# Optimization experiments

Measured on AMD Instinct MI355X. Metric: run time of the kernel, lower is better.

Reference implementation:

```python
import math
import jax, jax.numpy as jnp
import numpy as np

D_MODEL = 1024
NUM_HEADS = 16
HEAD_DIM = D_MODEL // NUM_HEADS
B, T = 2, 2048


def setup_inputs() -> dict:
    key = jax.random.key(0)
    ks = jax.random.split(key, 11)
    s = 0.02
    inp = {
        'x':  jax.random.normal(ks[0], (B, T, D_MODEL), dtype=jnp.float32),
        'Wq': jax.random.normal(ks[1], (D_MODEL, D_MODEL), dtype=jnp.float32) * s,
        'bq': jax.random.normal(ks[2], (D_MODEL,), dtype=jnp.float32) * s,
        'Wk': jax.random.normal(ks[3], (D_MODEL, D_MODEL), dtype=jnp.float32) * s,
        'bk': jax.random.normal(ks[4], (D_MODEL,), dtype=jnp.float32) * s,
        'Wv': jax.random.normal(ks[5], (D_MODEL, D_MODEL), dtype=jnp.float32) * s,
        'bv': jax.random.normal(ks[6], (D_MODEL,), dtype=jnp.float32) * s,
        'Wt': jax.random.normal(ks[7], (D_MODEL, D_MODEL), dtype=jnp.float32) * s,
        'bt': jax.random.normal(ks[8], (D_MODEL,), dtype=jnp.float32) * s,
        'Wo': jax.random.normal(ks[9], (D_MODEL, D_MODEL), dtype=jnp.float32) * s,
        'bo': jax.random.normal(ks[10], (D_MODEL,), dtype=jnp.float32) * s,
    }
    return inp


def reference(x, Wq, bq, Wk, bk, Wv, bv, Wt, bt, Wo, bo):
    Bx, Tx, D = x.shape
    H, hd = NUM_HEADS, HEAD_DIM
    scale = 1.0 / math.sqrt(hd)

    def proj(W, b):
        # (B,T,D) -> (B,H,T,hd); torch Linear uses x @ W.T + b
        return (x @ W.T + b).reshape(Bx, Tx, H, hd).transpose(0, 2, 1, 3)

    q = proj(Wq, bq)
    k = proj(Wk, bk)
    v = proj(Wv, bv)
    t = proj(Wt, bt)

    # dot-product term: (B,H,T,T)
    scores = jnp.einsum('bhqd,bhkd->bhqk', q, k)
    # triplet term: cumsum over key positions of (k*v)/sqrt(hd)
    kv_cumsum = jnp.cumsum(k * v * scale, axis=2)  # (B,H,T,hd)
    scores = scores + jnp.einsum('bhqd,bhkd->bhqk', q * t, kv_cumsum)
    scores = scores * scale

    # causal mask: position j > i forbidden
    causal = jnp.tril(jnp.ones((Tx, Tx), dtype=bool))
    scores = jnp.where(causal[None, None], scores, jnp.float32(-jnp.inf))

    attn = jax.nn.softmax(scores, axis=-1)  # stable max-subtract internally
    out = jnp.einsum('bhqk,bhkd->bhqd', attn, v)
    out = out.transpose(0, 2, 1, 3).reshape(Bx, Tx, D)
    return out @ Wo.T + bo
```

## Files before the change

kernel.cpp:

```cpp
#include <hip/hip_runtime.h>
#include <hip/hip_bf16.h>

typedef unsigned short u16;
typedef __attribute__((ext_vector_type(8))) short bf16x8;
typedef __attribute__((ext_vector_type(4))) float f32x4;
typedef __attribute__((ext_vector_type(4))) unsigned int u32x4;

#define LOG2E 1.44269504088896340736f

static __device__ __forceinline__ float b2f(u16 u) {
    union { float f; unsigned int i; } v; v.i = ((unsigned int)u) << 16; return v.f;
}
static __device__ __forceinline__ u16 f2b(float f) {
    unsigned int x = __builtin_bit_cast(unsigned int, f);
    unsigned int r = (x + 0x7fffu + ((x >> 16) & 1u)) >> 16;
    return (u16)r;
}
static __device__ __forceinline__ void gll16(const u16* g, u16* l) {
    __builtin_amdgcn_global_load_lds((const __attribute__((address_space(1))) void*)g,
                                     (__attribute__((address_space(3))) void*)l, 16, 0, 0);
}
static __device__ __forceinline__ float fexp2(float x) {
    float r; asm("v_exp_f32 %0, %1" : "=v"(r) : "v"(x)); return r;
}

__global__ __launch_bounds__(256) void cvt_all(const float* __restrict__ x,
                                               const float* __restrict__ w0, const float* __restrict__ w1,
                                               const float* __restrict__ w2, const float* __restrict__ w3,
                                               const float* __restrict__ w4, u16* __restrict__ dst) {
    size_t c = (size_t)blockIdx.x * 256 + threadIdx.x;
    size_t e = c * 4;
    const float* s; size_t off;
    const size_t M4 = (size_t)4 << 20, M1 = (size_t)1 << 20;
    if (e < M4) { s = x; off = e; }
    else {
        size_t r = e - M4; int wsel = (int)(r >> 20); off = r & (M1 - 1);
        s = wsel == 0 ? w0 : wsel == 1 ? w1 : wsel == 2 ? w2 : wsel == 3 ? w3 : w4;
    }
    float4 v = *(const float4*)(s + off);
    u16* d = dst + e;
    d[0] = f2b(v.x); d[1] = f2b(v.y); d[2] = f2b(v.z); d[3] = f2b(v.w);
}

static __device__ __forceinline__ void gemm_body(const u16* __restrict__ A, const u16* __restrict__ W,
                                                 const float* __restrict__ bias, void* __restrict__ outp,
                                                 int mode, u16* Al, u16* Bl) {
    const int tid = threadIdx.x, lane = tid & 63, w = tid >> 6;
    const int wr = w >> 1, wc = w & 1;
    const int l15 = lane & 15, lhi = lane >> 4;
    const int tm = blockIdx.y * 128, tn = blockIdx.x * 128;

    f32x4 acc[4][4] = {};

    for (int kt = 0; kt < 16; ++kt) {
        const int k0 = kt * 64;
        for (int i = 0; i < 4; ++i) {
            int rl = i * 32 + w * 8 + (lane >> 3);
            int c  = (lane & 7) ^ (rl & 7);
            gll16(A + (size_t)(tm + rl) * 1024 + k0 + c * 8, Al + (i * 32 + w * 8) * 64);
            gll16(W + (size_t)(tn + rl) * 1024 + k0 + c * 8, Bl + (i * 32 + w * 8) * 64);
        }
        __syncthreads();
        for (int ks = 0; ks < 2; ++ks) {
            bf16x8 af[4], bfr[4];
            for (int mi = 0; mi < 4; ++mi) {
                int row = wr * 64 + mi * 16 + l15;
                int cc = (ks * 4 + lhi) ^ (row & 7);
                af[mi] = *(const bf16x8*)(Al + row * 64 + cc * 8);
            }
            for (int ni = 0; ni < 4; ++ni) {
                int row = wc * 64 + ni * 16 + l15;
                int cc = (ks * 4 + lhi) ^ (row & 7);
                bfr[ni] = *(const bf16x8*)(Bl + row * 64 + cc * 8);
            }
            for (int mi = 0; mi < 4; ++mi)
                for (int ni = 0; ni < 4; ++ni)
                    acc[mi][ni] = __builtin_amdgcn_mfma_f32_16x16x32_bf16(af[mi], bfr[ni], acc[mi][ni], 0, 0, 0);
        }
        __syncthreads();
    }

    float bcol[4];
    for (int ni = 0; ni < 4; ++ni) bcol[ni] = bias[tn + wc * 64 + ni * 16 + l15];

    for (int mi = 0; mi < 4; ++mi)
        for (int ni = 0; ni < 4; ++ni)
            for (int r = 0; r < 4; ++r) {
                int rg = tm + wr * 64 + mi * 16 + lhi * 4 + r;
                int cg = tn + wc * 64 + ni * 16 + l15;
                float v = acc[mi][ni][r] + bcol[ni];
                if (mode == 2) {
                    ((float*)outp)[(size_t)rg * 1024 + cg] = v;
                } else {
                    int b = rg >> 11, t = rg & 2047, h = cg >> 6, d = cg & 63;
                    if (mode == 0)
                        ((u16*)outp)[(((size_t)(b * 16 + h)) * 2048 + t) * 128 + d] = f2b(v);
                    else
                        ((u16*)outp)[(((size_t)(b * 16 + h)) * 2048 + t) * 64 + d] = f2b(v);
                }
            }
}

__global__ __launch_bounds__(256) void gemm_bt(const u16* __restrict__ A, const u16* __restrict__ W,
                                               const float* __restrict__ bias, void* __restrict__ outp,
                                               int mode) {
    __shared__ u16 Al[128 * 64];
    __shared__ u16 Bl[128 * 64];
    gemm_body(A, W, bias, outp, mode, Al, Bl);
}

struct ProjArgs {
    const u16* W[4];
    const float* b[4];
    u16* out[4];
};

__global__ __launch_bounds__(256) void gemm_proj(const u16* __restrict__ A, ProjArgs pa) {
    __shared__ u16 Al[128 * 64];
    __shared__ u16 Bl[128 * 64];
    const int z = blockIdx.z;
    gemm_body(A, pa.W[z], pa.b[z], pa.out[z], (z < 2) ? 0 : 1, Al, Bl);
}

__global__ __launch_bounds__(256) void qt_mul(u16* __restrict__ Qa, const u16* __restrict__ Tp) {
    int idx = blockIdx.x * 256 + threadIdx.x;
    int tg = idx >> 3, dc = idx & 7;
    bf16x8 q = *(const bf16x8*)(Qa + (size_t)tg * 128 + dc * 8);
    bf16x8 tt = *(const bf16x8*)(Tp + (size_t)tg * 64 + dc * 8);
    bf16x8 o;
    #pragma unroll
    for (int j = 0; j < 8; ++j) o[j] = (short)f2b(b2f((u16)q[j]) * b2f((u16)tt[j]));
    *(bf16x8*)(Qa + (size_t)tg * 128 + 64 + dc * 8) = o;
}

__global__ __launch_bounds__(256) void transpose_v(const u16* __restrict__ V, u16* __restrict__ VT) {
    __shared__ u16 tile[64][72];
    const int bh = blockIdx.y, tc = blockIdx.x;
    const u16* Vh = V + ((size_t)bh * 2048 + tc * 64) * 64;
    u16* VTh = VT + (size_t)bh * 64 * 2048 + tc * 64;
    const int tid = threadIdx.x;
    for (int i = 0; i < 2; ++i) {
        int f = i * 256 + tid;
        int r = f >> 3, dc = f & 7;
        bf16x8 v = *(const bf16x8*)(Vh + r * 64 + dc * 8);
        #pragma unroll
        for (int j = 0; j < 8; ++j) tile[dc * 8 + j][r] = (u16)v[j];
    }
    __syncthreads();
    for (int i = 0; i < 2; ++i) {
        int f = i * 256 + tid;
        int d = f >> 3, t8 = (f & 7) * 8;
        bf16x8 o;
        #pragma unroll
        for (int j = 0; j < 8; ++j) {
            int pos = t8 + j;
            int key = (pos & 32) + 16 * ((pos >> 2) & 1) + 4 * ((pos >> 3) & 3) + (pos & 3);
            o[j] = (short)tile[d][key];
        }
        *(bf16x8*)(VTh + (size_t)d * 2048 + t8) = o;
    }
}

__global__ __launch_bounds__(256) void cumsum_kv(u16* __restrict__ Ka, const u16* __restrict__ V) {
    const int bh = blockIdx.x, dg = blockIdx.y;
    u16* Kh = Ka + (size_t)bh * 2048 * 128;
    const u16* Vh = V + (size_t)bh * 2048 * 64;
    const int d16 = threadIdx.x & 15, c = threadIdx.x >> 4;
    const int d = dg * 16 + d16;
    __shared__ float sums[16][17];
    float s = 0.f;
    for (int i = 0; i < 128; ++i) {
        int t = c * 128 + i;
        s += b2f(Kh[t * 128 + d]) * b2f(Vh[t * 64 + d]);
    }
    sums[c][d16] = s;
    __syncthreads();
    float run = 0.f;
    for (int cc = 0; cc < c; ++cc) run += sums[cc][d16];
    for (int i = 0; i < 128; ++i) {
        int t = c * 128 + i;
        run += b2f(Kh[t * 128 + d]) * b2f(Vh[t * 64 + d]);
        Kh[t * 128 + 64 + d] = f2b(run * 0.125f);
    }
}

__global__ __launch_bounds__(256, 3) void attn5(const u16* __restrict__ Qa, const u16* __restrict__ Ka,
                                                const u16* __restrict__ VT, u16* __restrict__ Obuf) {
    const int wg = blockIdx.x;
    const int xcd = wg & 7, slot = wg >> 3;
    const int bh = xcd * 4 + (slot >> 4);
    const int qp = slot & 15;
    const int tiL = qp, tiH = 31 - qp;
    const int q0L = tiL * 64, q0H = tiH * 64;
    const int NT = tiH + 1;
    const u16* Qh = Qa + (size_t)bh * 2048 * 128;
    const u16* Kh = Ka + (size_t)bh * 2048 * 128;
    const u16* VTh = VT + (size_t)bh * 64 * 2048;

    __shared__ u16 Kl[2][64 * 128];
    __shared__ u16 Vl[2][64 * 64];

    const int tid = threadIdx.x, lane = tid & 63, w = tid >> 6;
    const int l15 = lane & 15, lhi = lane >> 4;
    const float SC = 0.125f * LOG2E;

    bf16x8 qfL[4], qfH[4];
    #pragma unroll
    for (int ks = 0; ks < 4; ++ks) {
        bf16x8 a = *(const bf16x8*)(Qh + (size_t)(q0L + w * 16 + l15) * 128 + ks * 32 + lhi * 8);
        bf16x8 b = *(const bf16x8*)(Qh + (size_t)(q0H + w * 16 + l15) * 128 + ks * 32 + lhi * 8);
        bf16x8 oa, ob;
        #pragma unroll
        for (int j = 0; j < 8; ++j) {
            oa[j] = (short)f2b(b2f((u16)a[j]) * SC);
            ob[j] = (short)f2b(b2f((u16)b[j]) * SC);
        }
        qfL[ks] = oa; qfH[ks] = ob;
    }

    f32x4 accL[4] = {}, accH[4] = {};
    float lsL = 0.f, lsH = 0.f;

    auto STAGE = [&](int buf, int ti) {
        const int kv0 = ti * 64;
        #pragma unroll
        for (int i = 0; i < 4; ++i) {
            int lr = i * 16 + w * 4 + lhi;
            int c = l15 ^ (lr & 15);
            gll16(Kh + (size_t)(kv0 + lr) * 128 + c * 8, &Kl[buf][(i * 16 + w * 4) * 128]);
        }
        #pragma unroll
        for (int i = 0; i < 2; ++i) {
            int dr = i * 32 + w * 8 + (lane >> 3);
            int c = (lane & 7) ^ (dr & 7);
            gll16(VTh + (size_t)dr * 2048 + kv0 + c * 8, &Vl[buf][(i * 32 + w * 8) * 64]);
        }
    };

    STAGE(0, 0);
    asm volatile("s_waitcnt vmcnt(0)" ::: "memory");
    __builtin_amdgcn_s_barrier();

    for (int ti = 0; ti < NT; ++ti) {
        const int cur = ti & 1;
        if (ti + 1 < NT) STAGE(cur ^ 1, ti + 1);
        const bool doL = (ti <= tiL);

        f32x4 sH[4] = {}, sL[4] = {};
        #pragma unroll
        for (int ks = 0; ks < 4; ++ks) {
            bf16x8 kf[4];
            #pragma unroll
            for (int k2 = 0; k2 < 4; ++k2) {
                int kl = k2 * 16 + l15;
                int cc = (ks * 4 + lhi) ^ l15;
                kf[k2] = *(const bf16x8*)(&Kl[cur][kl * 128 + cc * 8]);
            }
            __builtin_amdgcn_s_setprio(1);
            #pragma unroll
            for (int k2 = 0; k2 < 4; ++k2)
                sH[k2] = __builtin_amdgcn_mfma_f32_16x16x32_bf16(kf[k2], qfH[ks], sH[k2], 0, 0, 0);
            if (doL) {
                #pragma unroll
                for (int k2 = 0; k2 < 4; ++k2)
                    sL[k2] = __builtin_amdgcn_mfma_f32_16x16x32_bf16(kf[k2], qfL[ks], sL[k2], 0, 0, 0);
            }
            __builtin_amdgcn_s_setprio(0);
        }

        auto FINISH = [&](f32x4* sacc, f32x4* acc, float& lsum, bool diag) {
            float p[4][4];
            #pragma unroll
            for (int k2 = 0; k2 < 4; ++k2)
                #pragma unroll
                for (int r = 0; r < 4; ++r) {
                    float s = sacc[k2][r];
                    if (diag) {
                        int key = k2 * 16 + lhi * 4 + r;
                        int qq = w * 16 + l15;
                        s = (key <= qq) ? s : -1e30f;
                    }
                    float pe = fexp2(s);
                    p[k2][r] = pe;
                    lsum += pe;
                }
            bf16x8 pf[2];
            #pragma unroll
            for (int ks2 = 0; ks2 < 2; ++ks2) {
                unsigned int w0, w1, w2, w3;
                asm("v_cvt_pk_bf16_f32 %0, %1, %2" : "=v"(w0) : "v"(p[2 * ks2][0]),     "v"(p[2 * ks2][1]));
                asm("v_cvt_pk_bf16_f32 %0, %1, %2" : "=v"(w1) : "v"(p[2 * ks2][2]),     "v"(p[2 * ks2][3]));
                asm("v_cvt_pk_bf16_f32 %0, %1, %2" : "=v"(w2) : "v"(p[2 * ks2 + 1][0]), "v"(p[2 * ks2 + 1][1]));
                asm("v_cvt_pk_bf16_f32 %0, %1, %2" : "=v"(w3) : "v"(p[2 * ks2 + 1][2]), "v"(p[2 * ks2 + 1][3]));
                u32x4 t = {w0, w1, w2, w3};
                pf[ks2] = __builtin_bit_cast(bf16x8, t);
            }
            #pragma unroll
            for (int ks2 = 0; ks2 < 2; ++ks2) {
                __builtin_amdgcn_s_setprio(1);
                #pragma unroll
                for (int dt = 0; dt < 4; ++dt) {
                    int dd = dt * 16 + l15;
                    int cc = (ks2 * 4 + lhi) ^ (dd & 7);
                    bf16x8 vf = *(const bf16x8*)(&Vl[cur][dd * 64 + cc * 8]);
                    acc[dt] = __builtin_amdgcn_mfma_f32_16x16x32_bf16(pf[ks2], vf, acc[dt], 0, 0, 0);
                }
                __builtin_amdgcn_s_setprio(0);
            }
        };

        FINISH(sH, accH, lsH, ti == tiH);
        if (doL) FINISH(sL, accL, lsL, ti == tiL);

        asm volatile("s_waitcnt vmcnt(0)" ::: "memory");
        __builtin_amdgcn_s_barrier();
    }

    lsH += __shfl_xor(lsH, 16, 64); lsH += __shfl_xor(lsH, 32, 64);
    lsL += __shfl_xor(lsL, 16, 64); lsL += __shfl_xor(lsL, 32, 64);
    float invH[4], invL[4];
    #pragma unroll
    for (int r = 0; r < 4; ++r) {
        invH[r] = 1.0f / __shfl(lsH, lhi * 4 + r, 64);
        invL[r] = 1.0f / __shfl(lsL, lhi * 4 + r, 64);
    }
    #pragma unroll
    for (int dt = 0; dt < 4; ++dt)
        #pragma unroll
        for (int r = 0; r < 4; ++r) {
            int cr = lhi * 4 + r;
            int dd = dt * 16 + l15;
            int qgL = q0L + w * 16 + cr;
            int qgH = q0H + w * 16 + cr;
            size_t nL = (size_t)(bh >> 4) * 2048 + qgL;
            size_t nH = (size_t)(bh >> 4) * 2048 + qgH;
            Obuf[nL * 1024 + (bh & 15) * 64 + dd] = f2b(accL[dt][r] * invL[r]);
            Obuf[nH * 1024 + (bh & 15) * 64 + dd] = f2b(accH[dt][r] * invH[r]);
        }
}

extern "C" void kernel_launch(void* const* d_in, const int* in_sizes, int n_in,
                              void* d_out, int out_size, void* d_ws, size_t ws_size,
                              hipStream_t stream) {
    (void)in_sizes; (void)n_in; (void)out_size; (void)ws_size;
    const float* x  = (const float*)d_in[0];
    const float* Wq = (const float*)d_in[1];
    const float* bq = (const float*)d_in[2];
    const float* Wk = (const float*)d_in[3];
    const float* bk = (const float*)d_in[4];
    const float* Wv = (const float*)d_in[5];
    const float* bv = (const float*)d_in[6];
    const float* Wt = (const float*)d_in[7];
    const float* bt = (const float*)d_in[8];
    const float* Wo = (const float*)d_in[9];
    const float* bo = (const float*)d_in[10];

    const size_t M1 = 1024u * 1024u;
    u16* xb   = (u16*)d_ws;
    u16* wq   = xb + 4 * M1;
    u16* wk   = wq + M1;
    u16* wv   = wk + M1;
    u16* wt   = wv + M1;
    u16* wo   = wt + M1;
    u16* Qa   = wo + M1;
    u16* Kaa  = Qa + 8 * M1;
    u16* Vtm  = Kaa + 8 * M1;
    u16* Ttm  = Vtm + 4 * M1;
    u16* Obuf = Ttm + 4 * M1;
    u16* VTg  = Ttm;

    cvt_all<<<9216, 256, 0, stream>>>(x, Wq, Wk, Wv, Wt, Wo, xb);

    ProjArgs pa;
    pa.W[0] = wq; pa.W[1] = wk; pa.W[2] = wv; pa.W[3] = wt;
    pa.b[0] = bq; pa.b[1] = bk; pa.b[2] = bv; pa.b[3] = bt;
    pa.out[0] = Qa; pa.out[1] = Kaa; pa.out[2] = Vtm; pa.out[3] = Ttm;
    gemm_proj<<<dim3(8, 32, 4), 256, 0, stream>>>(xb, pa);

    qt_mul<<<2048, 256, 0, stream>>>(Qa, Ttm);
    transpose_v<<<dim3(32, 32), 256, 0, stream>>>(Vtm, VTg);
    cumsum_kv<<<dim3(32, 4), 256, 0, stream>>>(Kaa, Vtm);

    attn5<<<512, 256, 0, stream>>>(Qa, Kaa, VTg, Obuf);

    gemm_bt<<<dim3(8, 32), 256, 0, stream>>>(Obuf, wo, bo, d_out, 2);
}
```

Before: 158.1 us.

## Split attention into 32-row query pairs with 2-wave blocks, load V directly to registers

The attention kernel moves from 4-wave blocks handling paired 64-row query tiles to 2-wave blocks handling paired 32-row tiles, doubling the grid to 1024 blocks. V fragments are now read straight from global memory into registers each tile instead of being staged through LDS, and the wait/barrier is adjusted to allow partial vmcnt overlap. The output projection now uses a 64x128 tile, giving twice as many blocks. The aim is better CU occupancy and load balance on this small problem, at the cost of more redundant K loads per query row and uncoalesced V reads.

```diff
diff --git a/kernel.cpp b/kernel.cpp
--- a/kernel.cpp
+++ b/kernel.cpp
@@ -42,38 +42,50 @@
     d[0] = f2b(v.x); d[1] = f2b(v.y); d[2] = f2b(v.z); d[3] = f2b(v.w);
 }
 
+template<int WM>
 static __device__ __forceinline__ void gemm_body(const u16* __restrict__ A, const u16* __restrict__ W,
                                                  const float* __restrict__ bias, void* __restrict__ outp,
                                                  int mode, u16* Al, u16* Bl) {
     const int tid = threadIdx.x, lane = tid & 63, w = tid >> 6;
     const int wr = w >> 1, wc = w & 1;
     const int l15 = lane & 15, lhi = lane >> 4;
-    const int tm = blockIdx.y * 128, tn = blockIdx.x * 128;
-
-    f32x4 acc[4][4] = {};
+    const int tm = blockIdx.y * (WM * 32), tn = blockIdx.x * 128;
+
+    f32x4 acc[WM][4] = {};
 
     for (int kt = 0; kt < 16; ++kt) {
         const int k0 = kt * 64;
+        #pragma unroll
+        for (int i = 0; i < WM; ++i) {
+            int rl = i * 32 + w * 8 + (lane >> 3);
+            int c  = (lane & 7) ^ (rl & 7);
+            gll16(A + (size_t)(tm + rl) * 1024 + k0 + c * 8, Al + (i * 32 + w * 8) * 64);
+        }
+        #pragma unroll
         for (int i = 0; i < 4; ++i) {
             int rl = i * 32 + w * 8 + (lane >> 3);
             int c  = (lane & 7) ^ (rl & 7);
-            gll16(A + (size_t)(tm + rl) * 1024 + k0 + c * 8, Al + (i * 32 + w * 8) * 64);
             gll16(W + (size_t)(tn + rl) * 1024 + k0 + c * 8, Bl + (i * 32 + w * 8) * 64);
         }
         __syncthreads();
+        #pragma unroll
         for (int ks = 0; ks < 2; ++ks) {
-            bf16x8 af[4], bfr[4];
-            for (int mi = 0; mi < 4; ++mi) {
-                int row = wr * 64 + mi * 16 + l15;
+            bf16x8 af[WM], bfr[4];
+            #pragma unroll
+            for (int mi = 0; mi < WM; ++mi) {
+                int row = wr * (WM * 16) + mi * 16 + l15;
                 int cc = (ks * 4 + lhi) ^ (row & 7);
                 af[mi] = *(const bf16x8*)(Al + row * 64 + cc * 8);
             }
+            #pragma unroll
             for (int ni = 0; ni < 4; ++ni) {
                 int row = wc * 64 + ni * 16 + l15;
                 int cc = (ks * 4 + lhi) ^ (row & 7);
                 bfr[ni] = *(const bf16x8*)(Bl + row * 64 + cc * 8);
             }
-            for (int mi = 0; mi < 4; ++mi)
+            #pragma unroll
+            for (int mi = 0; mi < WM; ++mi)
+                #pragma unroll
                 for (int ni = 0; ni < 4; ++ni)
                     acc[mi][ni] = __builtin_amdgcn_mfma_f32_16x16x32_bf16(af[mi], bfr[ni], acc[mi][ni], 0, 0, 0);
         }
@@ -81,12 +93,16 @@
     }
 
     float bcol[4];
+    #pragma unroll
     for (int ni = 0; ni < 4; ++ni) bcol[ni] = bias[tn + wc * 64 + ni * 16 + l15];
 
-    for (int mi = 0; mi < 4; ++mi)
+    #pragma unroll
+    for (int mi = 0; mi < WM; ++mi)
+        #pragma unroll
         for (int ni = 0; ni < 4; ++ni)
+            #pragma unroll
             for (int r = 0; r < 4; ++r) {
-                int rg = tm + wr * 64 + mi * 16 + lhi * 4 + r;
+                int rg = tm + wr * (WM * 16) + mi * 16 + lhi * 4 + r;
                 int cg = tn + wc * 64 + ni * 16 + l15;
                 float v = acc[mi][ni][r] + bcol[ni];
                 if (mode == 2) {
@@ -101,14 +117,6 @@
             }
 }
 
-__global__ __launch_bounds__(256) void gemm_bt(const u16* __restrict__ A, const u16* __restrict__ W,
-                                               const float* __restrict__ bias, void* __restrict__ outp,
-                                               int mode) {
-    __shared__ u16 Al[128 * 64];
-    __shared__ u16 Bl[128 * 64];
-    gemm_body(A, W, bias, outp, mode, Al, Bl);
-}
-
 struct ProjArgs {
     const u16* W[4];
     const float* b[4];
@@ -119,7 +127,14 @@
     __shared__ u16 Al[128 * 64];
     __shared__ u16 Bl[128 * 64];
     const int z = blockIdx.z;
-    gemm_body(A, pa.W[z], pa.b[z], pa.out[z], (z < 2) ? 0 : 1, Al, Bl);
+    gemm_body<4>(A, pa.W[z], pa.b[z], pa.out[z], (z < 2) ? 0 : 1, Al, Bl);
+}
+
+__global__ __launch_bounds__(256) void gemm_out2(const u16* __restrict__ A, const u16* __restrict__ W,
+                                                 const float* __restrict__ bias, void* __restrict__ out) {
+    __shared__ u16 Al[64 * 64];
+    __shared__ u16 Bl[128 * 64];
+    gemm_body<2>(A, W, bias, out, 2, Al, Bl);
 }
 
 __global__ __launch_bounds__(256) void qt_mul(u16* __restrict__ Qa, const u16* __restrict__ Tp) {
@@ -184,21 +199,21 @@
     }
 }
 
-__global__ __launch_bounds__(256, 3) void attn5(const u16* __restrict__ Qa, const u16* __restrict__ Ka,
-                                                const u16* __restrict__ VT, u16* __restrict__ Obuf) {
+__global__ __launch_bounds__(128) void attn6(const u16* __restrict__ Qa, const u16* __restrict__ Ka,
+                                             const u16* __restrict__ VT, u16* __restrict__ Obuf) {
     const int wg = blockIdx.x;
     const int xcd = wg & 7, slot = wg >> 3;
-    const int bh = xcd * 4 + (slot >> 4);
-    const int qp = slot & 15;
-    const int tiL = qp, tiH = 31 - qp;
-    const int q0L = tiL * 64, q0H = tiH * 64;
-    const int NT = tiH + 1;
+    const int bh = xcd * 4 + (slot >> 5);
+    const int qp = slot & 31;
+    const int hiq = 63 - qp, loq = qp;
+    const int q0H = hiq * 32, q0L = loq * 32;
+    const int NT = (hiq >> 1) + 1;
+    const int lastL = loq >> 1;
     const u16* Qh = Qa + (size_t)bh * 2048 * 128;
     const u16* Kh = Ka + (size_t)bh * 2048 * 128;
     const u16* VTh = VT + (size_t)bh * 64 * 2048;
 
     __shared__ u16 Kl[2][64 * 128];
-    __shared__ u16 Vl[2][64 * 64];
 
     const int tid = threadIdx.x, lane = tid & 63, w = tid >> 6;
     const int l15 = lane & 15, lhi = lane >> 4;
@@ -221,31 +236,36 @@
     f32x4 accL[4] = {}, accH[4] = {};
     float lsL = 0.f, lsH = 0.f;
 
-    auto STAGE = [&](int buf, int ti) {
+    auto STAGEK = [&](int buf, int ti) {
         const int kv0 = ti * 64;
         #pragma unroll
-        for (int i = 0; i < 4; ++i) {
-            int lr = i * 16 + w * 4 + lhi;
+        for (int i = 0; i < 8; ++i) {
+            int lr = i * 8 + w * 4 + lhi;
             int c = l15 ^ (lr & 15);
-            gll16(Kh + (size_t)(kv0 + lr) * 128 + c * 8, &Kl[buf][(i * 16 + w * 4) * 128]);
-        }
-        #pragma unroll
-        for (int i = 0; i < 2; ++i) {
-            int dr = i * 32 + w * 8 + (lane >> 3);
-            int c = (lane & 7) ^ (dr & 7);
-            gll16(VTh + (size_t)dr * 2048 + kv0 + c * 8, &Vl[buf][(i * 32 + w * 8) * 64]);
+            gll16(Kh + (size_t)(kv0 + lr) * 128 + c * 8, &Kl[buf][(i * 8 + w * 4) * 128]);
         }
     };
 
-    STAGE(0, 0);
+    STAGEK(0, 0);
     asm volatile("s_waitcnt vmcnt(0)" ::: "memory");
     __builtin_amdgcn_s_barrier();
 
     for (int ti = 0; ti < NT; ++ti) {
         const int cur = ti & 1;
-        if (ti + 1 < NT) STAGE(cur ^ 1, ti + 1);
-        const bool doL = (ti <= tiL);
-
+        const int kv0 = ti * 64;
+
+        bf16x8 vf[2][4];
+        #pragma unroll
+        for (int ks2 = 0; ks2 < 2; ++ks2)
+            #pragma unroll
+            for (int dt = 0; dt < 4; ++dt)
+                vf[ks2][dt] = *(const bf16x8*)(VTh + (size_t)(dt * 16 + l15) * 2048 + kv0 + (ks2 * 4 + lhi) * 8);
+
+        const bool haveStage = (ti + 1 < NT);
+        if (haveStage) STAGEK(cur ^ 1, ti + 1);
+        asm volatile("" ::: "memory");
+
+        const bool doL = (ti <= lastL);
         f32x4 sH[4] = {}, sL[4] = {};
         #pragma unroll
         for (int ks = 0; ks < 4; ++ks) {
@@ -268,7 +288,10 @@
             __builtin_amdgcn_s_setprio(0);
         }
 
-        auto FINISH = [&](f32x4* sacc, f32x4* acc, float& lsum, bool diag) {
+        if (haveStage) asm volatile("s_waitcnt vmcnt(8)" ::: "memory");
+        else           asm volatile("s_waitcnt vmcnt(0)" ::: "memory");
+
+        auto FINISH = [&](f32x4* sacc, f32x4* acc, float& lsum, bool diag, int q0) {
             float p[4][4];
             #pragma unroll
             for (int k2 = 0; k2 < 4; ++k2)
@@ -276,8 +299,8 @@
                 for (int r = 0; r < 4; ++r) {
                     float s = sacc[k2][r];
                     if (diag) {
-                        int key = k2 * 16 + lhi * 4 + r;
-                        int qq = w * 16 + l15;
+                        int key = kv0 + k2 * 16 + lhi * 4 + r;
+                        int qq = q0 + w * 16 + l15;
                         s = (key <= qq) ? s : -1e30f;
                     }
                     float pe = fexp2(s);
@@ -299,21 +322,19 @@
             for (int ks2 = 0; ks2 < 2; ++ks2) {
                 __builtin_amdgcn_s_setprio(1);
                 #pragma unroll
-                for (int dt = 0; dt < 4; ++dt) {
-                    int dd = dt * 16 + l15;
-                    int cc = (ks2 * 4 + lhi) ^ (dd & 7);
-                    bf16x8 vf = *(const bf16x8*)(&Vl[cur][dd * 64 + cc * 8]);
-                    acc[dt] = __builtin_amdgcn_mfma_f32_16x16x32_bf16(pf[ks2], vf, acc[dt], 0, 0, 0);
-                }
+                for (int dt = 0; dt < 4; ++dt)
+                    acc[dt] = __builtin_amdgcn_mfma_f32_16x16x32_bf16(pf[ks2], vf[ks2][dt], acc[dt], 0, 0, 0);
                 __builtin_amdgcn_s_setprio(0);
             }
         };
 
-        FINISH(sH, accH, lsH, ti == tiH);
-        if (doL) FINISH(sL, accL, lsL, ti == tiL);
-
-        asm volatile("s_waitcnt vmcnt(0)" ::: "memory");
-        __builtin_amdgcn_s_barrier();
+        FINISH(sH, accH, lsH, ti == NT - 1, q0H);
+        if (doL) FINISH(sL, accL, lsL, ti == lastL, q0L);
+
+        if (haveStage) {
+            asm volatile("s_waitcnt vmcnt(0)" ::: "memory");
+            __builtin_amdgcn_s_barrier();
+        }
     }
 
     lsH += __shfl_xor(lsH, 16, 64); lsH += __shfl_xor(lsH, 32, 64);
@@ -381,7 +402,7 @@
     transpose_v<<<dim3(32, 32), 256, 0, stream>>>(Vtm, VTg);
     cumsum_kv<<<dim3(32, 4), 256, 0, stream>>>(Kaa, Vtm);
 
-    attn5<<<512, 256, 0, stream>>>(Qa, Kaa, VTg, Obuf);
-
-    gemm_bt<<<dim3(8, 32), 256, 0, stream>>>(Obuf, wo, bo, d_out, 2);
-}
+    attn6<<<1024, 128, 0, stream>>>(Qa, Kaa, VTg, Obuf);
+
+    gemm_out2<<<dim3(8, 64), 256, 0, stream>>>(Obuf, wo, bo, d_out);
+}
```

After: 188.0 us. 18.9% more time.

## Fuse small elementwise kernels and use smaller M tiles for output GEMM

Applied to the files above, without the earlier changes.

Three small kernels (q*t multiply, V transpose, KV cumsum) are merged into one launch whose work is picked by block index. This cuts launch overhead and lets the three pieces run at the same time; VT now reuses the xb buffer so it does not alias Ttm while q*t reads it. The cumsum part is reworked to use 4-wide vector loads with shorter 32-step chunks across 64 threads. The output projection GEMM is templated to 64-row tiles, giving 512 blocks for better CU occupancy on the small final GEMM.

```diff
diff --git a/kernel.cpp b/kernel.cpp
--- a/kernel.cpp
+++ b/kernel.cpp
@@ -42,38 +42,50 @@
     d[0] = f2b(v.x); d[1] = f2b(v.y); d[2] = f2b(v.z); d[3] = f2b(v.w);
 }
 
+template<int WM>
 static __device__ __forceinline__ void gemm_body(const u16* __restrict__ A, const u16* __restrict__ W,
                                                  const float* __restrict__ bias, void* __restrict__ outp,
                                                  int mode, u16* Al, u16* Bl) {
     const int tid = threadIdx.x, lane = tid & 63, w = tid >> 6;
     const int wr = w >> 1, wc = w & 1;
     const int l15 = lane & 15, lhi = lane >> 4;
-    const int tm = blockIdx.y * 128, tn = blockIdx.x * 128;
-
-    f32x4 acc[4][4] = {};
+    const int tm = blockIdx.y * (WM * 32), tn = blockIdx.x * 128;
+
+    f32x4 acc[WM][4] = {};
 
     for (int kt = 0; kt < 16; ++kt) {
         const int k0 = kt * 64;
+        #pragma unroll
+        for (int i = 0; i < WM; ++i) {
+            int rl = i * 32 + w * 8 + (lane >> 3);
+            int c  = (lane & 7) ^ (rl & 7);
+            gll16(A + (size_t)(tm + rl) * 1024 + k0 + c * 8, Al + (i * 32 + w * 8) * 64);
+        }
+        #pragma unroll
         for (int i = 0; i < 4; ++i) {
             int rl = i * 32 + w * 8 + (lane >> 3);
             int c  = (lane & 7) ^ (rl & 7);
-            gll16(A + (size_t)(tm + rl) * 1024 + k0 + c * 8, Al + (i * 32 + w * 8) * 64);
             gll16(W + (size_t)(tn + rl) * 1024 + k0 + c * 8, Bl + (i * 32 + w * 8) * 64);
         }
         __syncthreads();
+        #pragma unroll
         for (int ks = 0; ks < 2; ++ks) {
-            bf16x8 af[4], bfr[4];
-            for (int mi = 0; mi < 4; ++mi) {
-                int row = wr * 64 + mi * 16 + l15;
+            bf16x8 af[WM], bfr[4];
+            #pragma unroll
+            for (int mi = 0; mi < WM; ++mi) {
+                int row = wr * (WM * 16) + mi * 16 + l15;
                 int cc = (ks * 4 + lhi) ^ (row & 7);
                 af[mi] = *(const bf16x8*)(Al + row * 64 + cc * 8);
             }
+            #pragma unroll
             for (int ni = 0; ni < 4; ++ni) {
                 int row = wc * 64 + ni * 16 + l15;
                 int cc = (ks * 4 + lhi) ^ (row & 7);
                 bfr[ni] = *(const bf16x8*)(Bl + row * 64 + cc * 8);
             }
-            for (int mi = 0; mi < 4; ++mi)
+            #pragma unroll
+            for (int mi = 0; mi < WM; ++mi)
+                #pragma unroll
                 for (int ni = 0; ni < 4; ++ni)
                     acc[mi][ni] = __builtin_amdgcn_mfma_f32_16x16x32_bf16(af[mi], bfr[ni], acc[mi][ni], 0, 0, 0);
         }
@@ -81,12 +93,16 @@
     }
 
     float bcol[4];
+    #pragma unroll
     for (int ni = 0; ni < 4; ++ni) bcol[ni] = bias[tn + wc * 64 + ni * 16 + l15];
 
-    for (int mi = 0; mi < 4; ++mi)
+    #pragma unroll
+    for (int mi = 0; mi < WM; ++mi)
+        #pragma unroll
         for (int ni = 0; ni < 4; ++ni)
+            #pragma unroll
             for (int r = 0; r < 4; ++r) {
-                int rg = tm + wr * 64 + mi * 16 + lhi * 4 + r;
+                int rg = tm + wr * (WM * 16) + mi * 16 + lhi * 4 + r;
                 int cg = tn + wc * 64 + ni * 16 + l15;
                 float v = acc[mi][ni][r] + bcol[ni];
                 if (mode == 2) {
@@ -101,14 +117,6 @@
             }
 }
 
-__global__ __launch_bounds__(256) void gemm_bt(const u16* __restrict__ A, const u16* __restrict__ W,
-                                               const float* __restrict__ bias, void* __restrict__ outp,
-                                               int mode) {
-    __shared__ u16 Al[128 * 64];
-    __shared__ u16 Bl[128 * 64];
-    gemm_body(A, W, bias, outp, mode, Al, Bl);
-}
-
 struct ProjArgs {
     const u16* W[4];
     const float* b[4];
@@ -119,68 +127,96 @@
     __shared__ u16 Al[128 * 64];
     __shared__ u16 Bl[128 * 64];
     const int z = blockIdx.z;
-    gemm_body(A, pa.W[z], pa.b[z], pa.out[z], (z < 2) ? 0 : 1, Al, Bl);
-}
-
-__global__ __launch_bounds__(256) void qt_mul(u16* __restrict__ Qa, const u16* __restrict__ Tp) {
-    int idx = blockIdx.x * 256 + threadIdx.x;
-    int tg = idx >> 3, dc = idx & 7;
-    bf16x8 q = *(const bf16x8*)(Qa + (size_t)tg * 128 + dc * 8);
-    bf16x8 tt = *(const bf16x8*)(Tp + (size_t)tg * 64 + dc * 8);
-    bf16x8 o;
-    #pragma unroll
-    for (int j = 0; j < 8; ++j) o[j] = (short)f2b(b2f((u16)q[j]) * b2f((u16)tt[j]));
-    *(bf16x8*)(Qa + (size_t)tg * 128 + 64 + dc * 8) = o;
-}
-
-__global__ __launch_bounds__(256) void transpose_v(const u16* __restrict__ V, u16* __restrict__ VT) {
-    __shared__ u16 tile[64][72];
-    const int bh = blockIdx.y, tc = blockIdx.x;
-    const u16* Vh = V + ((size_t)bh * 2048 + tc * 64) * 64;
-    u16* VTh = VT + (size_t)bh * 64 * 2048 + tc * 64;
-    const int tid = threadIdx.x;
-    for (int i = 0; i < 2; ++i) {
-        int f = i * 256 + tid;
-        int r = f >> 3, dc = f & 7;
-        bf16x8 v = *(const bf16x8*)(Vh + r * 64 + dc * 8);
-        #pragma unroll
-        for (int j = 0; j < 8; ++j) tile[dc * 8 + j][r] = (u16)v[j];
-    }
-    __syncthreads();
-    for (int i = 0; i < 2; ++i) {
-        int f = i * 256 + tid;
-        int d = f >> 3, t8 = (f & 7) * 8;
+    gemm_body<4>(A, pa.W[z], pa.b[z], pa.out[z], (z < 2) ? 0 : 1, Al, Bl);
+}
+
+__global__ __launch_bounds__(256) void gemm_out2(const u16* __restrict__ A, const u16* __restrict__ W,
+                                                 const float* __restrict__ bias, void* __restrict__ out) {
+    __shared__ u16 Al[64 * 64];
+    __shared__ u16 Bl[128 * 64];
+    gemm_body<2>(A, W, bias, out, 2, Al, Bl);
+}
+
+__global__ __launch_bounds__(256) void fuse_small(u16* __restrict__ Qa, const u16* __restrict__ Tp,
+                                                  const u16* __restrict__ V, u16* __restrict__ VT,
+                                                  u16* __restrict__ Ka) {
+    __shared__ char shmem[64 * 72 * 2];
+    const int b = blockIdx.x, tid = threadIdx.x;
+
+    if (b < 2048) {
+        int idx = b * 256 + tid;
+        int tg = idx >> 3, dc = idx & 7;
+        bf16x8 q = *(const bf16x8*)(Qa + (size_t)tg * 128 + dc * 8);
+        bf16x8 tt = *(const bf16x8*)(Tp + (size_t)tg * 64 + dc * 8);
         bf16x8 o;
         #pragma unroll
-        for (int j = 0; j < 8; ++j) {
-            int pos = t8 + j;
-            int key = (pos & 32) + 16 * ((pos >> 2) & 1) + 4 * ((pos >> 3) & 3) + (pos & 3);
-            o[j] = (short)tile[d][key];
-        }
-        *(bf16x8*)(VTh + (size_t)d * 2048 + t8) = o;
-    }
-}
-
-__global__ __launch_bounds__(256) void cumsum_kv(u16* __restrict__ Ka, const u16* __restrict__ V) {
-    const int bh = blockIdx.x, dg = blockIdx.y;
-    u16* Kh = Ka + (size_t)bh * 2048 * 128;
-    const u16* Vh = V + (size_t)bh * 2048 * 64;
-    const int d16 = threadIdx.x & 15, c = threadIdx.x >> 4;
-    const int d = dg * 16 + d16;
-    __shared__ float sums[16][17];
-    float s = 0.f;
-    for (int i = 0; i < 128; ++i) {
-        int t = c * 128 + i;
-        s += b2f(Kh[t * 128 + d]) * b2f(Vh[t * 64 + d]);
-    }
-    sums[c][d16] = s;
-    __syncthreads();
-    float run = 0.f;
-    for (int cc = 0; cc < c; ++cc) run += sums[cc][d16];
-    for (int i = 0; i < 128; ++i) {
-        int t = c * 128 + i;
-        run += b2f(Kh[t * 128 + d]) * b2f(Vh[t * 64 + d]);
-        Kh[t * 128 + 64 + d] = f2b(run * 0.125f);
+        for (int j = 0; j < 8; ++j) o[j] = (short)f2b(b2f((u16)q[j]) * b2f((u16)tt[j]));
+        *(bf16x8*)(Qa + (size_t)tg * 128 + 64 + dc * 8) = o;
+    } else if (b < 3072) {
+        u16 (*tile)[72] = (u16(*)[72])shmem;
+        const int r0 = b - 2048;
+        const int bh = r0 >> 5, tc = r0 & 31;
+        const u16* Vh = V + ((size_t)bh * 2048 + tc * 64) * 64;
+        u16* VTh = VT + (size_t)bh * 64 * 2048 + tc * 64;
+        for (int i = 0; i < 2; ++i) {
+            int f = i * 256 + tid;
+            int r = f >> 3, dc = f & 7;
+            bf16x8 v = *(const bf16x8*)(Vh + r * 64 + dc * 8);
+            #pragma unroll
+            for (int j = 0; j < 8; ++j) tile[dc * 8 + j][r] = (u16)v[j];
+        }
+        __syncthreads();
+        for (int i = 0; i < 2; ++i) {
+            int f = i * 256 + tid;
+            int d = f >> 3, t8 = (f & 7) * 8;
+            bf16x8 o;
+            #pragma unroll
+            for (int j = 0; j < 8; ++j) {
+                int pos = t8 + j;
+                int key = (pos & 32) + 16 * ((pos >> 2) & 1) + 4 * ((pos >> 3) & 3) + (pos & 3);
+                o[j] = (short)tile[d][key];
+            }
+            *(bf16x8*)(VTh + (size_t)d * 2048 + t8) = o;
+        }
+    } else {
+        float4* sums = (float4*)shmem;
+        const int r0 = b - 3072;
+        const int bh = r0 & 31, dg = r0 >> 5;
+        u16* Kh = Ka + (size_t)bh * 2048 * 128;
+        const u16* Vh = V + (size_t)bh * 2048 * 64;
+        const int quad = tid & 3, c = tid >> 2;
+        const int d0 = dg * 16 + quad * 4;
+        float s0 = 0.f, s1 = 0.f, s2 = 0.f, s3 = 0.f;
+        for (int i = 0; i < 32; ++i) {
+            int t = c * 32 + i;
+            ushort4 kv = *(const ushort4*)(Kh + (size_t)t * 128 + d0);
+            ushort4 vv = *(const ushort4*)(Vh + (size_t)t * 64 + d0);
+            s0 += b2f(kv.x) * b2f(vv.x);
+            s1 += b2f(kv.y) * b2f(vv.y);
+            s2 += b2f(kv.z) * b2f(vv.z);
+            s3 += b2f(kv.w) * b2f(vv.w);
+        }
+        float4 sv; sv.x = s0; sv.y = s1; sv.z = s2; sv.w = s3;
+        sums[c * 4 + quad] = sv;
+        __syncthreads();
+        float4 run; run.x = run.y = run.z = run.w = 0.f;
+        for (int cc = 0; cc < c; ++cc) {
+            float4 ss = sums[cc * 4 + quad];
+            run.x += ss.x; run.y += ss.y; run.z += ss.z; run.w += ss.w;
+        }
+        for (int i = 0; i < 32; ++i) {
+            int t = c * 32 + i;
+            ushort4 kv = *(const ushort4*)(Kh + (size_t)t * 128 + d0);
+            ushort4 vv = *(const ushort4*)(Vh + (size_t)t * 64 + d0);
+            run.x += b2f(kv.x) * b2f(vv.x);
+            run.y += b2f(kv.y) * b2f(vv.y);
+            run.z += b2f(kv.z) * b2f(vv.z);
+            run.w += b2f(kv.w) * b2f(vv.w);
+            ushort4 o;
+            o.x = f2b(run.x * 0.125f); o.y = f2b(run.y * 0.125f);
+            o.z = f2b(run.z * 0.125f); o.w = f2b(run.w * 0.125f);
+            *(ushort4*)(Kh + (size_t)t * 128 + 64 + d0) = o;
+        }
     }
 }
 
@@ -367,7 +403,7 @@
     u16* Vtm  = Kaa + 8 * M1;
     u16* Ttm  = Vtm + 4 * M1;
     u16* Obuf = Ttm + 4 * M1;
-    u16* VTg  = Ttm;
+    u16* VTg  = xb;
 
     cvt_all<<<9216, 256, 0, stream>>>(x, Wq, Wk, Wv, Wt, Wo, xb);
 
@@ -377,11 +413,9 @@
     pa.out[0] = Qa; pa.out[1] = Kaa; pa.out[2] = Vtm; pa.out[3] = Ttm;
     gemm_proj<<<dim3(8, 32, 4), 256, 0, stream>>>(xb, pa);
 
-    qt_mul<<<2048, 256, 0, stream>>>(Qa, Ttm);
-    transpose_v<<<dim3(32, 32), 256, 0, stream>>>(Vtm, VTg);
-    cumsum_kv<<<dim3(32, 4), 256, 0, stream>>>(Kaa, Vtm);
+    fuse_small<<<3200, 256, 0, stream>>>(Qa, Ttm, Vtm, VTg, Kaa);
 
     attn5<<<512, 256, 0, stream>>>(Qa, Kaa, VTg, Obuf);
 
-    gemm_bt<<<dim3(8, 32), 256, 0, stream>>>(Obuf, wo, bo, d_out, 2);
-}
+    gemm_out2<<<dim3(8, 64), 256, 0, stream>>>(Obuf, wo, bo, d_out);
+}
```

Result: faster. 145.7 us (-7.8%).
